# Performance work log

Measured on AMD Instinct MI355X. Metric: run time of the kernel, lower is better.

The kernel has to match this reference:

```python
import jax, jax.numpy as jnp
import numpy as np

N_NODES = 50000
N_EDGES = 800000
IN_DIM = 128
HID_DIM = 128


def _gcn_norm(edge_index, num_nodes):
    # Add self-loops, then symmetric normalization D^-1/2 (A+I) D^-1/2
    loop = jnp.arange(num_nodes, dtype=edge_index.dtype)
    row = jnp.concatenate([edge_index[0], loop])  # source nodes
    col = jnp.concatenate([edge_index[1], loop])  # target nodes
    ew = jnp.ones(row.shape[0], dtype=jnp.float32)
    deg = jax.ops.segment_sum(ew, col, num_segments=num_nodes)
    dinv = jnp.where(deg > 0, jax.lax.rsqrt(deg), 0.0)
    norm = dinv[row] * ew * dinv[col]
    return row, col, norm


def _gcn_layer(h, row, col, norm, W, b, num_nodes):
    h = h @ W                              # [N, D] linear transform first
    msg = h[row] * norm[:, None]           # gather + normalize  [E+N, D]
    out = jax.ops.segment_sum(msg, col, num_segments=num_nodes)  # scatter-add
    return out + b


def setup_inputs() -> dict:
    key = jax.random.key(0)
    k1, k2, k3, k4 = jax.random.split(key, 4)
    x = jax.random.normal(k1, (N_NODES, IN_DIM), dtype=jnp.float32)
    edge_index = jax.random.randint(k2, (2, N_EDGES), 0, N_NODES, dtype=jnp.int32)
    W1 = jax.random.normal(k3, (IN_DIM, HID_DIM), dtype=jnp.float32) * (1.0 / np.sqrt(IN_DIM))
    b1 = jnp.zeros((HID_DIM,), dtype=jnp.float32)
    W2 = jax.random.normal(k4, (HID_DIM, HID_DIM), dtype=jnp.float32) * (1.0 / np.sqrt(HID_DIM))
    b2 = jnp.zeros((HID_DIM,), dtype=jnp.float32)
    return {"x": x, "edge_index": edge_index, "W1": W1, "b1": b1, "W2": W2, "b2": b2}


def reference(x, edge_index, W1, b1, W2, b2):
    n = x.shape[0]
    row, col, norm = _gcn_norm(edge_index, n)
    z = _gcn_layer(x, row, col, norm, W1, b1, n)
    z = jax.nn.relu(z)
    z = _gcn_layer(z, row, col, norm, W2, b2, n)
    z = jax.nn.relu(z)
    return z
```

## Files before the change

kernel.cpp:

```cpp
#include <hip/hip_runtime.h>
#include <hip/hip_bf16.h>
#include <hip/hip_fp16.h>


#define BK 128
#define CAP 4096
#define PACK_ROWBITS 20
#define NB_MAX 512
#define CHUNK 2048

typedef __attribute__((ext_vector_type(4))) _Float16 f16x4;
typedef __attribute__((ext_vector_type(4))) float f32x4;

__global__ __launch_bounds__(256) void k_bscatter(const int* __restrict__ row,
                                                  const int* __restrict__ col,
                                                  int* gcur, unsigned* ebuf,
                                                  int E, int nb) {
    __shared__ int h[NB_MAX];
    __shared__ int base[NB_MAX];
    const int t = threadIdx.x;
    const int e0 = blockIdx.x * CHUNK;
    int cs[CHUNK / 256];
    for (int i = t; i < nb; i += 256) h[i] = 0;
    __syncthreads();
#pragma unroll
    for (int q = 0; q < CHUNK / 256; q++) {
        int e = e0 + q * 256 + t;
        cs[q] = (e < E) ? col[e] : -1;
        if (cs[q] >= 0) atomicAdd(&h[cs[q] >> 7], 1);
    }
    __syncthreads();
    for (int i = t; i < nb; i += 256) {
        base[i] = h[i] ? atomicAdd(&gcur[i], h[i]) : 0;
        h[i] = 0;
    }
    __syncthreads();
#pragma unroll
    for (int q = 0; q < CHUNK / 256; q++) {
        int e = e0 + q * 256 + t;
        if (cs[q] >= 0) {
            int c = cs[q];
            int b = c >> 7;
            int loc = atomicAdd(&h[b], 1);
            ebuf[b * CAP + base[b] + loc] =
                (unsigned)row[e] | ((unsigned)(c & (BK - 1)) << PACK_ROWBITS);
        }
    }
}

__global__ __launch_bounds__(256) void k_bnodefill(const unsigned* __restrict__ ebuf,
                                                   const int* __restrict__ gcur,
                                                   int* degi, float* dinv, int* startv,
                                                   int* srcs, int N) {
    __shared__ int h[BK];
    __shared__ int sc[BK];
    const int t = threadIdx.x, b = blockIdx.x;
    const int s = b * CAP;
    const int cnt = gcur[b];
    if (t < BK) h[t] = 0;
    __syncthreads();
    for (int i = t; i < cnt; i += 256)
        atomicAdd(&h[(ebuf[s + i] >> PACK_ROWBITS) & (BK - 1)], 1);
    __syncthreads();
    int deg = (t < BK) ? h[t] : 0;
    if (t < BK) sc[t] = deg;
    __syncthreads();
    for (int o = 1; o < BK; o <<= 1) {
        int x = (t < BK && t >= o) ? sc[t - o] : 0;
        __syncthreads();
        if (t < BK) sc[t] += x;
        __syncthreads();
    }
    int node = b * BK + t;
    if (t < BK) {
        int lexcl = sc[t] - deg;
        if (node < N) {
            degi[node]   = deg;
            dinv[node]   = rsqrtf((float)deg + 1.0f);
            startv[node] = s + lexcl;
        }
        h[t] = lexcl;
    }
    __syncthreads();
    for (int i = t; i < cnt; i += 256) {
        unsigned u = ebuf[s + i];
        int c = (u >> PACK_ROWBITS) & (BK - 1);
        int loc = atomicAdd(&h[c], 1);
        srcs[s + loc] = (int)(u & ((1u << PACK_ROWBITS) - 1));
    }
}

template <typename TIN>
__global__ __launch_bounds__(256) void k_gemm(const TIN* __restrict__ A,
                                              const float* __restrict__ W,
                                              __half* __restrict__ C, int M) {
    __shared__ _Float16 Wt[128][136];
    const int t = threadIdx.x;
    for (int idx = t; idx < 4096; idx += 256) {
        int k = idx >> 5, n4 = (idx & 31) << 2;
        float4 w4 = ((const float4*)W)[idx];
        Wt[n4 + 0][k] = (_Float16)w4.x;
        Wt[n4 + 1][k] = (_Float16)w4.y;
        Wt[n4 + 2][k] = (_Float16)w4.z;
        Wt[n4 + 3][k] = (_Float16)w4.w;
    }
    __syncthreads();

    const int wave = t >> 6, lane = t & 63;
    const int l16 = lane & 15, g = lane >> 4;
    const int rbase = blockIdx.x * 64 + wave * 16;
    int r = rbase + l16;
    if (r >= M) r = M - 1;

    f32x4 acc[8];
#pragma unroll
    for (int ct = 0; ct < 8; ct++) acc[ct] = (f32x4){0.f, 0.f, 0.f, 0.f};

#pragma unroll
    for (int s = 0; s < 8; s++) {
        const int k0 = s * 16 + g * 4;
        f16x4 a;
        if constexpr (sizeof(TIN) == 4) {
            float4 a4 = *(const float4*)((const float*)A + (size_t)r * 128 + k0);
            a = (f16x4){(_Float16)a4.x, (_Float16)a4.y, (_Float16)a4.z, (_Float16)a4.w};
        } else {
            a = *(const f16x4*)((const _Float16*)A + (size_t)r * 128 + k0);
        }
#pragma unroll
        for (int ct = 0; ct < 8; ct++) {
            f16x4 b = *(const f16x4*)(&Wt[ct * 16 + l16][k0]);
            acc[ct] = __builtin_amdgcn_mfma_f32_16x16x16f16(a, b, acc[ct], 0, 0, 0);
        }
    }

#pragma unroll
    for (int ct = 0; ct < 8; ct++) {
#pragma unroll
        for (int i = 0; i < 4; i++) {
            int rr = rbase + g * 4 + i;
            if (rr < M)
                C[(size_t)rr * 128 + ct * 16 + l16] = __float2half(acc[ct][i]);
        }
    }
}

__global__ __launch_bounds__(256) void k_agg(const __half* __restrict__ H,
                                             const int* __restrict__ srcs,
                                             const int* __restrict__ startv,
                                             const int* __restrict__ degi,
                                             const float* __restrict__ dinv,
                                             const float* __restrict__ bias,
                                             float* __restrict__ outF,
                                             __half* __restrict__ outH, int n) {
    int wave = threadIdx.x >> 6, lane = threadIdx.x & 63;
    int node = blockIdx.x * 4 + wave;
    if (node >= n) return;
    int s0 = startv[node];
    int d = degi[node];
    float di = dinv[node];
    const __half2* Hv = (const __half2*)H;

    float2 hv = __half22float2(Hv[(size_t)node * 64 + lane]);
    float ax = di * hv.x, ay = di * hv.y;

    for (int k = 0; k < d; k += 64) {
        int take = d - k; if (take > 64) take = 64;
        int idx = (lane < take) ? srcs[s0 + k + lane] : node;
        float djl = (lane < take) ? dinv[idx] : 0.f;
        for (int u = 0; u < take; u += 8) {
            int jj[8]; float dd[8]; float2 vv[8];
#pragma unroll
            for (int q = 0; q < 8; q++) {
                jj[q] = __shfl(idx, u + q);
                dd[q] = __shfl(djl, u + q);
            }
#pragma unroll
            for (int q = 0; q < 8; q++) vv[q] = __half22float2(Hv[(size_t)jj[q] * 64 + lane]);
#pragma unroll
            for (int q = 0; q < 8; q++) {
                ax = fmaf(dd[q], vv[q].x, ax);
                ay = fmaf(dd[q], vv[q].y, ay);
            }
        }
    }
    float2 b2 = ((const float2*)bias)[lane];
    float ox = fmaxf(fmaf(di, ax, b2.x), 0.f);
    float oy = fmaxf(fmaf(di, ay, b2.y), 0.f);
    if (outF) {
        ((float2*)outF)[(size_t)node * 64 + lane] = make_float2(ox, oy);
    } else {
        __half2 p = __floats2half2_rn(ox, oy);
        ((__half2*)outH)[(size_t)node * 64 + lane] = p;
    }
}

extern "C" void kernel_launch(void* const* d_in, const int* in_sizes, int n_in,
                              void* d_out, int out_size, void* d_ws, size_t ws_size,
                              hipStream_t stream) {
    const float* x  = (const float*)d_in[0];
    const int*   ei = (const int*)d_in[1];
    const float* W1 = (const float*)d_in[2];
    const float* b1 = (const float*)d_in[3];
    const float* W2 = (const float*)d_in[4];
    const float* b2 = (const float*)d_in[5];
    const int N = in_sizes[0] / 128;
    const int E = in_sizes[1] / 2;
    const int NB = (N + BK - 1) / BK;

    char* w = (char*)d_ws;
    auto alloc = [&](size_t bytes) -> void* {
        void* p = (void*)w;
        w += (bytes + 255) & ~(size_t)255;
        return p;
    };
    int*      degi     = (int*)alloc((size_t)N * 4);
    float*    dinv     = (float*)alloc((size_t)N * 4);
    int*      startv   = (int*)alloc((size_t)N * 4);
    int*      gcur     = (int*)alloc((size_t)NB * 4);
    unsigned* ebuf     = (unsigned*)alloc((size_t)NB * CAP * 4);
    int*      srcs     = (int*)alloc((size_t)NB * CAP * 4);
    __half*   H        = (__half*)alloc((size_t)N * 128 * 2);
    __half*   Z        = (__half*)alloc((size_t)N * 128 * 2);

    const int* rowp = ei;
    const int* colp = ei + E;
    const int nScatter = (E + CHUNK - 1) / CHUNK;

    (void)hipMemsetAsync(gcur, 0, (size_t)NB * 4, stream);
    k_bscatter<<<nScatter, 256, 0, stream>>>(rowp, colp, gcur, ebuf, E, NB);
    k_bnodefill<<<NB, 256, 0, stream>>>(ebuf, gcur, degi, dinv, startv, srcs, N);

    k_gemm<float><<<(N + 63) / 64, 256, 0, stream>>>(x, W1, H, N);
    k_agg<<<(N + 3) / 4, 256, 0, stream>>>(H, srcs, startv, degi, dinv, b1,
                                           nullptr, Z, N);
    k_gemm<__half><<<(N + 63) / 64, 256, 0, stream>>>(Z, W2, H, N);
    k_agg<<<(N + 3) / 4, 256, 0, stream>>>(H, srcs, startv, degi, dinv, b2,
                                           (float*)d_out, nullptr, N);
}
```

Before: 149.0 us.

## Co-schedule edge bucketing with first GEMM in one launch; widen gather batch

Merges the edge bucket-scatter kernel and the first-layer GEMM into one horizontally fused launch. Block indices pick which role each block plays, and the shared memory is a union sized for either role. This removes one launch and lets the two independent workloads fill the GPU together. Separately, the aggregation inner loop now issues 16 neighbor row loads per batch instead of 8, for more memory-level parallelism. The cost is more registers per lane in the aggregation kernel, which may lower occupancy.

```diff
diff --git a/kernel.cpp b/kernel.cpp
--- a/kernel.cpp
+++ b/kernel.cpp
@@ -12,38 +12,91 @@
 typedef __attribute__((ext_vector_type(4))) _Float16 f16x4;
 typedef __attribute__((ext_vector_type(4))) float f32x4;
 
-__global__ __launch_bounds__(256) void k_bscatter(const int* __restrict__ row,
-                                                  const int* __restrict__ col,
-                                                  int* gcur, unsigned* ebuf,
-                                                  int E, int nb) {
-    __shared__ int h[NB_MAX];
-    __shared__ int base[NB_MAX];
+__global__ __launch_bounds__(256) void k_fused(const int* __restrict__ row,
+                                               const int* __restrict__ col,
+                                               int* gcur, unsigned* ebuf,
+                                               int E, int nb,
+                                               const float* __restrict__ A,
+                                               const float* __restrict__ W,
+                                               __half* __restrict__ C, int M,
+                                               int nScat) {
+    __shared__ union {
+        struct { int h[NB_MAX]; int base[NB_MAX]; } sc;
+        _Float16 Wt[128][136];
+    } u;
     const int t = threadIdx.x;
-    const int e0 = blockIdx.x * CHUNK;
-    int cs[CHUNK / 256];
-    for (int i = t; i < nb; i += 256) h[i] = 0;
-    __syncthreads();
-#pragma unroll
-    for (int q = 0; q < CHUNK / 256; q++) {
-        int e = e0 + q * 256 + t;
-        cs[q] = (e < E) ? col[e] : -1;
-        if (cs[q] >= 0) atomicAdd(&h[cs[q] >> 7], 1);
-    }
-    __syncthreads();
-    for (int i = t; i < nb; i += 256) {
-        base[i] = h[i] ? atomicAdd(&gcur[i], h[i]) : 0;
-        h[i] = 0;
-    }
-    __syncthreads();
-#pragma unroll
-    for (int q = 0; q < CHUNK / 256; q++) {
-        int e = e0 + q * 256 + t;
-        if (cs[q] >= 0) {
-            int c = cs[q];
-            int b = c >> 7;
-            int loc = atomicAdd(&h[b], 1);
-            ebuf[b * CAP + base[b] + loc] =
-                (unsigned)row[e] | ((unsigned)(c & (BK - 1)) << PACK_ROWBITS);
+
+    if (blockIdx.x < nScat) {
+        const int e0 = blockIdx.x * CHUNK;
+        int cs[CHUNK / 256];
+        for (int i = t; i < nb; i += 256) u.sc.h[i] = 0;
+        __syncthreads();
+#pragma unroll
+        for (int q = 0; q < CHUNK / 256; q++) {
+            int e = e0 + q * 256 + t;
+            cs[q] = (e < E) ? col[e] : -1;
+            if (cs[q] >= 0) atomicAdd(&u.sc.h[cs[q] >> 7], 1);
+        }
+        __syncthreads();
+        for (int i = t; i < nb; i += 256) {
+            u.sc.base[i] = u.sc.h[i] ? atomicAdd(&gcur[i], u.sc.h[i]) : 0;
+            u.sc.h[i] = 0;
+        }
+        __syncthreads();
+#pragma unroll
+        for (int q = 0; q < CHUNK / 256; q++) {
+            int e = e0 + q * 256 + t;
+            if (cs[q] >= 0) {
+                int c = cs[q];
+                int b = c >> 7;
+                int loc = atomicAdd(&u.sc.h[b], 1);
+                ebuf[b * CAP + u.sc.base[b] + loc] =
+                    (unsigned)row[e] | ((unsigned)(c & (BK - 1)) << PACK_ROWBITS);
+            }
+        }
+    } else {
+        const int bid = blockIdx.x - nScat;
+        for (int idx = t; idx < 4096; idx += 256) {
+            int k = idx >> 5, n4 = (idx & 31) << 2;
+            float4 w4 = ((const float4*)W)[idx];
+            u.Wt[n4 + 0][k] = (_Float16)w4.x;
+            u.Wt[n4 + 1][k] = (_Float16)w4.y;
+            u.Wt[n4 + 2][k] = (_Float16)w4.z;
+            u.Wt[n4 + 3][k] = (_Float16)w4.w;
+        }
+        __syncthreads();
+
+        const int wave = t >> 6, lane = t & 63;
+        const int l16 = lane & 15, g = lane >> 4;
+        const int rbase = bid * 64 + wave * 16;
+        int r = rbase + l16;
+        if (r >= M) r = M - 1;
+
+        f32x4 acc[8];
+#pragma unroll
+        for (int ct = 0; ct < 8; ct++) acc[ct] = (f32x4){0.f, 0.f, 0.f, 0.f};
+
+#pragma unroll
+        for (int s = 0; s < 8; s++) {
+            const int k0 = s * 16 + g * 4;
+            float4 a4 = *(const float4*)(A + (size_t)r * 128 + k0);
+            f16x4 a = (f16x4){(_Float16)a4.x, (_Float16)a4.y,
+                              (_Float16)a4.z, (_Float16)a4.w};
+#pragma unroll
+            for (int ct = 0; ct < 8; ct++) {
+                f16x4 b = *(const f16x4*)(&u.Wt[ct * 16 + l16][k0]);
+                acc[ct] = __builtin_amdgcn_mfma_f32_16x16x16f16(a, b, acc[ct], 0, 0, 0);
+            }
+        }
+
+#pragma unroll
+        for (int ct = 0; ct < 8; ct++) {
+#pragma unroll
+            for (int i = 0; i < 4; i++) {
+                int rr = rbase + g * 4 + i;
+                if (rr < M)
+                    C[(size_t)rr * 128 + ct * 16 + l16] = __float2half(acc[ct][i]);
+            }
         }
     }
 }
@@ -90,10 +143,9 @@
     }
 }
 
-template <typename TIN>
-__global__ __launch_bounds__(256) void k_gemm(const TIN* __restrict__ A,
-                                              const float* __restrict__ W,
-                                              __half* __restrict__ C, int M) {
+__global__ __launch_bounds__(256) void k_gemm2(const __half* __restrict__ A,
+                                               const float* __restrict__ W,
+                                               __half* __restrict__ C, int M) {
     __shared__ _Float16 Wt[128][136];
     const int t = threadIdx.x;
     for (int idx = t; idx < 4096; idx += 256) {
@@ -119,13 +171,7 @@
 #pragma unroll
     for (int s = 0; s < 8; s++) {
         const int k0 = s * 16 + g * 4;
-        f16x4 a;
-        if constexpr (sizeof(TIN) == 4) {
-            float4 a4 = *(const float4*)((const float*)A + (size_t)r * 128 + k0);
-            a = (f16x4){(_Float16)a4.x, (_Float16)a4.y, (_Float16)a4.z, (_Float16)a4.w};
-        } else {
-            a = *(const f16x4*)((const _Float16*)A + (size_t)r * 128 + k0);
-        }
+        f16x4 a = *(const f16x4*)((const _Float16*)A + (size_t)r * 128 + k0);
 #pragma unroll
         for (int ct = 0; ct < 8; ct++) {
             f16x4 b = *(const f16x4*)(&Wt[ct * 16 + l16][k0]);
@@ -167,17 +213,17 @@
         int take = d - k; if (take > 64) take = 64;
         int idx = (lane < take) ? srcs[s0 + k + lane] : node;
         float djl = (lane < take) ? dinv[idx] : 0.f;
-        for (int u = 0; u < take; u += 8) {
-            int jj[8]; float dd[8]; float2 vv[8];
-#pragma unroll
-            for (int q = 0; q < 8; q++) {
+        for (int u = 0; u < take; u += 16) {
+            int jj[16]; float dd[16]; float2 vv[16];
+#pragma unroll
+            for (int q = 0; q < 16; q++) {
                 jj[q] = __shfl(idx, u + q);
                 dd[q] = __shfl(djl, u + q);
             }
 #pragma unroll
-            for (int q = 0; q < 8; q++) vv[q] = __half22float2(Hv[(size_t)jj[q] * 64 + lane]);
-#pragma unroll
-            for (int q = 0; q < 8; q++) {
+            for (int q = 0; q < 16; q++) vv[q] = __half22float2(Hv[(size_t)jj[q] * 64 + lane]);
+#pragma unroll
+            for (int q = 0; q < 16; q++) {
                 ax = fmaf(dd[q], vv[q].x, ax);
                 ay = fmaf(dd[q], vv[q].y, ay);
             }
@@ -224,16 +270,17 @@
 
     const int* rowp = ei;
     const int* colp = ei + E;
-    const int nScatter = (E + CHUNK - 1) / CHUNK;
+    const int nScat = (E + CHUNK - 1) / CHUNK;
+    const int nGemm = (N + 63) / 64;
 
     (void)hipMemsetAsync(gcur, 0, (size_t)NB * 4, stream);
-    k_bscatter<<<nScatter, 256, 0, stream>>>(rowp, colp, gcur, ebuf, E, NB);
+    k_fused<<<nScat + nGemm, 256, 0, stream>>>(rowp, colp, gcur, ebuf, E, NB,
+                                               x, W1, H, N, nScat);
     k_bnodefill<<<NB, 256, 0, stream>>>(ebuf, gcur, degi, dinv, startv, srcs, N);
 
-    k_gemm<float><<<(N + 63) / 64, 256, 0, stream>>>(x, W1, H, N);
     k_agg<<<(N + 3) / 4, 256, 0, stream>>>(H, srcs, startv, degi, dinv, b1,
                                            nullptr, Z, N);
-    k_gemm<__half><<<(N + 63) / 64, 256, 0, stream>>>(Z, W2, H, N);
+    k_gemm2<<<nGemm, 256, 0, stream>>>(Z, W2, H, N);
     k_agg<<<(N + 3) / 4, 256, 0, stream>>>(H, srcs, startv, degi, dinv, b2,
                                            (float*)d_out, nullptr, N);
 }
```

Measured after the change: 145.5 us. 1.02x faster.
